# Kernel optimization log

Hardware: AMD Instinct MI355X
Metric: run time of the kernel (lower is better)

The kernel has to match this reference:

```python
import jax, jax.numpy as jnp
import numpy as np

D_MODEL = 768
N_HEADS = 12
D_K = D_MODEL // N_HEADS
NEG = -1e9


def setup_inputs() -> dict:
    key = jax.random.key(0)
    ks = jax.random.split(key, 10)
    B, S = 2, 2048
    x = jax.random.normal(ks[0], (B, S, D_MODEL), dtype=jnp.float32)
    # causal mask, broadcastable over batch and heads
    mask = jnp.tril(jnp.ones((S, S), dtype=jnp.int32))[None, None]
    scale = 1.0 / np.sqrt(D_MODEL)
    def lin(k):
        return jax.random.normal(k, (D_MODEL, D_MODEL), dtype=jnp.float32) * scale
    return {
        "x": x, "mask": mask,
        "wq": lin(ks[1]), "bq": jnp.zeros((D_MODEL,), jnp.float32),
        "wk": lin(ks[2]), "bk": jnp.zeros((D_MODEL,), jnp.float32),
        "wv": lin(ks[3]), "bv": jnp.zeros((D_MODEL,), jnp.float32),
        "wo": lin(ks[4]), "bo": jnp.zeros((D_MODEL,), jnp.float32),
    }


def reference(x, mask, wq, bq, wk, bk, wv, bv, wo, bo):
    B, S, _ = x.shape
    def split_heads(t):  # [B,S,D] -> [B,H,S,dk]
        return t.reshape(B, S, N_HEADS, D_K).transpose(0, 2, 1, 3)
    q = split_heads(x @ wq + bq)
    k = split_heads(x @ wk + bk)
    v = split_heads(x @ wv + bv)
    scores = jnp.einsum("bhqd,bhkd->bhqk", q, k) / jnp.sqrt(jnp.float32(D_K))
    scores = jnp.where(mask == 0, NEG, scores)
    attn = jax.nn.softmax(scores, axis=-1)
    # dropout is identity in eval mode
    ctx = jnp.einsum("bhqk,bhkd->bhqd", attn, v)
    ctx = ctx.transpose(0, 2, 1, 3).reshape(B, S, D_MODEL)
    return ctx @ wo + bo
```

## Files before the change

kernel.cpp:

```cpp
#include <hip/hip_runtime.h>
#include <hip/hip_bf16.h>
#include <stdint.h>

#define DM   768
#define NH   12
#define DKH  64
#define BB   2
#define SS   2048
#define MT   (BB*SS)
#define NQKV (3*DM)

typedef __attribute__((ext_vector_type(8))) short short8;
typedef __attribute__((ext_vector_type(4))) float f32x4;

__device__ __forceinline__ unsigned short f2bf(float f) {
    union { float f; unsigned u; } v; v.f = f;
    unsigned r = v.u + 0x7fffu + ((v.u >> 16) & 1u);
    return (unsigned short)(r >> 16);
}

__device__ __forceinline__ void gload_lds16(const unsigned short* g, unsigned short* l) {
    __builtin_amdgcn_global_load_lds((const __attribute__((address_space(1))) void*)g,
                                     (__attribute__((address_space(3))) void*)l, 16, 0, 0);
}

__launch_bounds__(256)
__global__ void k_conv(const float* __restrict__ x, unsigned short* __restrict__ xb,
                       const float* __restrict__ wq, const float* __restrict__ wk,
                       const float* __restrict__ wv, const float* __restrict__ wo,
                       unsigned short* __restrict__ wT) {
    __shared__ float tile[32][33];
    const int t = threadIdx.x;
    if (blockIdx.x < 3072) {
        int i = blockIdx.x * 256 + t;
        const float4 v = ((const float4*)x)[i];
        ushort4 o;
        o.x = f2bf(v.x); o.y = f2bf(v.y); o.z = f2bf(v.z); o.w = f2bf(v.w);
        ((ushort4*)xb)[i] = o;
    } else {
        const int cid = blockIdx.x - 3072;
        const int sel = cid / 576;
        const int rem = cid - sel * 576;
        const int kb = rem / 24, nb = rem - (rem / 24) * 24;
        const float* w = (sel == 0) ? wq : (sel == 1) ? wk : (sel == 2) ? wv : wo;
        const int k0 = kb * 32, n0 = nb * 32;
        const int tx = t & 31, ty = t >> 5;
        #pragma unroll
        for (int j = 0; j < 4; j++)
            tile[ty + 8*j][tx] = w[(size_t)(k0 + ty + 8*j) * DM + n0 + tx];
        __syncthreads();
        #pragma unroll
        for (int j = 0; j < 4; j++)
            wT[(size_t)(sel*DM + n0 + ty + 8*j) * DM + k0 + tx] = f2bf(tile[tx][ty + 8*j]);
    }
}

__launch_bounds__(256, 3)
__global__ void k_gemm_qkv(const unsigned short* __restrict__ xb,
                           const unsigned short* __restrict__ wT,
                           const float* __restrict__ bq, const float* __restrict__ bk,
                           const float* __restrict__ bv,
                           unsigned short* __restrict__ Qb,
                           unsigned short* __restrict__ Kb,
                           unsigned short* __restrict__ Vt) {
    __shared__ __align__(16) unsigned short Sh[128*128];
    unsigned short* As = Sh;
    unsigned short* Bs = Sh + 128*64;
    const int t = threadIdx.x;
    const int m0 = blockIdx.x * 128;
    const int n0 = blockIdx.y * 128;
    const int wid = t >> 6, lane = t & 63, q4 = lane >> 4, l16 = lane & 15;
    const int wm = (wid >> 1) * 64, wn = (wid & 1) * 64;

    const int srow = lane >> 3;
    const int scol = ((lane & 7) ^ srow) * 8;
    const unsigned short* Ag = xb + (size_t)(m0 + wid*8 + srow) * DM + scol;
    const unsigned short* Bg = wT + (size_t)(n0 + wid*8 + srow) * DM + scol;
    unsigned short* ldsA = &As[(wid*8)*64];
    unsigned short* ldsB = &Bs[(wid*8)*64];
    const int swz = (l16 & 7) * 8;

    f32x4 acc[4][4];
    for (int i = 0; i < 4; i++) for (int j = 0; j < 4; j++)
        acc[i][j] = (f32x4){0.f, 0.f, 0.f, 0.f};

    for (int kt = 0; kt < DM; kt += 64) {
        #pragma unroll
        for (int j = 0; j < 4; j++) {
            gload_lds16(Ag + (size_t)(j*32) * DM + kt, ldsA + j*32*64);
            gload_lds16(Bg + (size_t)(j*32) * DM + kt, ldsB + j*32*64);
        }
        __syncthreads();
        #pragma unroll
        for (int kc = 0; kc < 2; kc++) {
            short8 af[4], bf[4];
            #pragma unroll
            for (int i = 0; i < 4; i++)
                af[i] = *(const short8*)&As[(wm + i*16 + l16)*64 + ((kc*32 + q4*8) ^ swz)];
            #pragma unroll
            for (int i = 0; i < 4; i++)
                bf[i] = *(const short8*)&Bs[(wn + i*16 + l16)*64 + ((kc*32 + q4*8) ^ swz)];
            #pragma unroll
            for (int mi = 0; mi < 4; mi++)
                #pragma unroll
                for (int ni = 0; ni < 4; ni++)
                    acc[mi][ni] = __builtin_amdgcn_mfma_f32_16x16x32_bf16(af[mi], bf[ni], acc[mi][ni], 0, 0, 0);
        }
        __syncthreads();
    }

    const int sel = n0 / DM;
    if (sel < 2) {
        const float* bias = (sel == 0) ? bq : bk;
        for (int ni = 0; ni < 4; ni++) {
            const int col = n0 + wn + ni*16 + l16;
            const int c = col - sel * DM;
            const float bsv = bias[c];
            const int h = c >> 6, d = c & 63;
            for (int mi = 0; mi < 4; mi++) {
                for (int r = 0; r < 4; r++) {
                    const int row = m0 + wm + mi*16 + q4*4 + r;
                    const int b = row >> 11, s = row & 2047;
                    const int bh = b * NH + h;
                    float v = acc[mi][ni][r] + bsv;
                    if (sel == 0) Qb[(bh*SS + s)*DKH + d] = f2bf(v * 0.18033688011112042f);
                    else          Kb[(bh*SS + s)*DKH + d] = f2bf(v);
                }
            }
        }
    } else {
        const int cbase = n0 - 2*DM;
        const int bb = m0 >> 11, sbase = m0 & 2047;
        #pragma unroll
        for (int ni = 0; ni < 4; ni++) {
            const int c = wn + ni*16 + l16;
            const float bsv = bv[cbase + c];
            #pragma unroll
            for (int mi = 0; mi < 4; mi++) {
                const int rowb = wm + mi*16 + q4*4;
                ushort4 o;
                o.x = f2bf(acc[mi][ni][0] + bsv);
                o.y = f2bf(acc[mi][ni][1] + bsv);
                o.z = f2bf(acc[mi][ni][2] + bsv);
                o.w = f2bf(acc[mi][ni][3] + bsv);
                *(ushort4*)&Sh[c*128 + (rowb ^ ((c & 7) * 8))] = o;
            }
        }
        __syncthreads();
        const int dr = t >> 1, sq = (t & 1) * 64;
        const int hh = (cbase + dr) >> 6, d = (cbase + dr) & 63;
        const int bh = bb * NH + hh;
        unsigned short* Vg = Vt + ((size_t)bh*DKH + d)*SS + sbase + sq;
        #pragma unroll
        for (int j = 0; j < 8; j++) {
            short8 v = *(const short8*)&Sh[dr*128 + ((sq + j*8) ^ ((dr & 7) * 8))];
            *(short8*)&Vg[j*8] = v;
        }
    }
}

__device__ const int UNITS[48] = {
  (15<<16)|(0<<8)|16, (31<<16)|(0<<8)|16, (31<<16)|(16<<8)|32, (30<<16)|(0<<8)|16,
  (14<<16)|(0<<8)|15, (29<<16)|(0<<8)|15, (29<<16)|(15<<8)|30, (28<<16)|(0<<8)|15, (30<<16)|(16<<8)|31,
  (13<<16)|(0<<8)|14, (27<<16)|(0<<8)|14, (27<<16)|(14<<8)|28, (26<<16)|(0<<8)|14, (28<<16)|(15<<8)|29,
  (12<<16)|(0<<8)|13, (25<<16)|(0<<8)|13, (25<<16)|(13<<8)|26, (24<<16)|(0<<8)|13, (26<<16)|(14<<8)|27,
  (11<<16)|(0<<8)|12, (23<<16)|(0<<8)|12, (23<<16)|(12<<8)|24, (22<<16)|(0<<8)|12, (24<<16)|(13<<8)|25,
  (10<<16)|(0<<8)|11, (21<<16)|(0<<8)|11, (21<<16)|(11<<8)|22, (20<<16)|(0<<8)|11, (22<<16)|(12<<8)|23,
  ( 9<<16)|(0<<8)|10, (19<<16)|(0<<8)|10, (19<<16)|(10<<8)|20, (18<<16)|(0<<8)|10, (20<<16)|(11<<8)|21,
  ( 8<<16)|(0<<8)| 9, (17<<16)|(0<<8)| 9, (17<<16)|( 9<<8)|18, (16<<16)|(0<<8)| 9, (18<<16)|(10<<8)|19,
  ( 7<<16)|(0<<8)| 8, (16<<16)|( 9<<8)|17,
  ( 6<<16)|(0<<8)| 7, ( 5<<16)|(0<<8)| 6, ( 4<<16)|(0<<8)| 5, ( 3<<16)|(0<<8)| 4,
  ( 2<<16)|(0<<8)| 3, ( 1<<16)|(0<<8)| 2, ( 0<<16)|(0<<8)| 1,
};

__launch_bounds__(256, 4)
__global__ void k_attn(const unsigned short* __restrict__ Qb,
                       const unsigned short* __restrict__ Kb,
                       const unsigned short* __restrict__ Vt,
                       unsigned short* __restrict__ ctx,
                       float* __restrict__ Opart, float* __restrict__ lpart) {
    __shared__ __align__(16) unsigned short Ks[2][64*64];
    __shared__ __align__(16) unsigned short Vs[2][64*64];
    const int t = threadIdx.x;
    const int wid = t >> 6, lane = t & 63, q4 = lane >> 4, l16 = lane & 15;

    const int lin = blockIdx.x;
    const int bh = lin % 24;
    const int info = UNITS[lin / 24];
    const int qblk = info >> 16, t0 = (info >> 8) & 0xff, t1 = info & 0xff;
    const int b = bh / NH, h = bh - b * NH;
    const int qw = qblk * 64 + wid * 16;

    const unsigned short* Qp = Qb + (size_t)bh * SS * DKH;
    const unsigned short* Kp = Kb + (size_t)bh * SS * DKH;
    const unsigned short* Vp = Vt + (size_t)bh * DKH * SS;

    const int grow = lane >> 3;
    const int gcol = ((lane & 7) ^ grow) * 8;
    const int swz  = (l16 & 7) * 8;

    short8 qf[2];
    qf[0] = *(const short8*)(Qp + (size_t)(qw + l16)*DKH +      q4*8);
    qf[1] = *(const short8*)(Qp + (size_t)(qw + l16)*DKH + 32 + q4*8);

    const short8 ones = (short8){(short)0x3F80, (short)0x3F80, (short)0x3F80, (short)0x3F80,
                                 (short)0x3F80, (short)0x3F80, (short)0x3F80, (short)0x3F80};

    f32x4 accO[4];
    #pragma unroll
    for (int j = 0; j < 4; j++) accO[j] = (f32x4){0.f, 0.f, 0.f, 0.f};
    f32x4 accL = (f32x4){0.f, 0.f, 0.f, 0.f};

    {
        const int kb0 = t0 * 64;
        #pragma unroll
        for (int jj = 0; jj < 2; jj++) {
            const int r0 = wid*16 + jj*8;
            gload_lds16(Kp + (size_t)(kb0 + r0 + grow)*DKH + gcol, &Ks[0][r0*64]);
            gload_lds16(Vp + (size_t)(r0 + grow)*SS + kb0 + gcol,  &Vs[0][r0*64]);
        }
    }
    asm volatile("s_waitcnt vmcnt(0)" ::: "memory");
    __syncthreads();

    for (int kt = t0; kt < t1; kt++) {
        const int cb = (kt - t0) & 1, nb = cb ^ 1;
        const bool hasN = (kt + 1 < t1);
        if (hasN) {
            const int kn = (kt + 1) * 64;
            #pragma unroll
            for (int jj = 0; jj < 2; jj++) {
                const int r0 = wid*16 + jj*8;
                gload_lds16(Kp + (size_t)(kn + r0 + grow)*DKH + gcol, &Ks[nb][r0*64]);
                gload_lds16(Vp + (size_t)(r0 + grow)*SS + kn + gcol,  &Vs[nb][r0*64]);
            }
        }
        f32x4 St[4];
        #pragma unroll
        for (int ni = 0; ni < 4; ni++) St[ni] = (f32x4){0.f, 0.f, 0.f, 0.f};
        __builtin_amdgcn_s_setprio(1);
        #pragma unroll
        for (int ni = 0; ni < 4; ni++) {
            const int rbase = (ni*16 + l16) * 64;
            short8 kf0 = *(const short8*)&Ks[cb][rbase + ((     q4*8) ^ swz)];
            short8 kf1 = *(const short8*)&Ks[cb][rbase + ((32 + q4*8) ^ swz)];
            St[ni] = __builtin_amdgcn_mfma_f32_16x16x32_bf16(kf0, qf[0], St[ni], 0, 0, 0);
            St[ni] = __builtin_amdgcn_mfma_f32_16x16x32_bf16(kf1, qf[1], St[ni], 0, 0, 0);
        }
        __builtin_amdgcn_s_setprio(0);
        float p[4][4];
        if (kt < qblk) {
            #pragma unroll
            for (int ni = 0; ni < 4; ni++)
                #pragma unroll
                for (int r = 0; r < 4; r++)
                    p[ni][r] = __builtin_amdgcn_exp2f(St[ni][r]);
        } else {
            const int qrow = qw + l16;
            #pragma unroll
            for (int ni = 0; ni < 4; ni++) {
                const int key0 = kt*64 + ni*16 + q4*4;
                #pragma unroll
                for (int r = 0; r < 4; r++)
                    p[ni][r] = (key0 + r > qrow) ? 0.f : __builtin_amdgcn_exp2f(St[ni][r]);
            }
        }
        union { short8 v; unsigned u[4]; } pf0, pf1;
        {
            union { __hip_bfloat162 v; unsigned u; } w;
            w.v = __float22bfloat162_rn(make_float2(p[0][0], p[0][1])); pf0.u[0] = w.u;
            w.v = __float22bfloat162_rn(make_float2(p[0][2], p[0][3])); pf0.u[1] = w.u;
            w.v = __float22bfloat162_rn(make_float2(p[1][0], p[1][1])); pf0.u[2] = w.u;
            w.v = __float22bfloat162_rn(make_float2(p[1][2], p[1][3])); pf0.u[3] = w.u;
            w.v = __float22bfloat162_rn(make_float2(p[2][0], p[2][1])); pf1.u[0] = w.u;
            w.v = __float22bfloat162_rn(make_float2(p[2][2], p[2][3])); pf1.u[1] = w.u;
            w.v = __float22bfloat162_rn(make_float2(p[3][0], p[3][1])); pf1.u[2] = w.u;
            w.v = __float22bfloat162_rn(make_float2(p[3][2], p[3][3])); pf1.u[3] = w.u;
        }
        __builtin_amdgcn_s_setprio(1);
        accL = __builtin_amdgcn_mfma_f32_16x16x32_bf16(ones, pf0.v, accL, 0, 0, 0);
        accL = __builtin_amdgcn_mfma_f32_16x16x32_bf16(ones, pf1.v, accL, 0, 0, 0);
        #pragma unroll
        for (int ndi = 0; ndi < 4; ndi++) {
            const int rbase = (ndi*16 + l16) * 64;
            union { short8 v; unsigned long long d[2]; } vf0, vf1;
            vf0.d[0] = *(const unsigned long long*)&Vs[cb][rbase + ((     q4*4) ^ swz)];
            vf0.d[1] = *(const unsigned long long*)&Vs[cb][rbase + ((16 + q4*4) ^ swz)];
            vf1.d[0] = *(const unsigned long long*)&Vs[cb][rbase + ((32 + q4*4) ^ swz)];
            vf1.d[1] = *(const unsigned long long*)&Vs[cb][rbase + ((48 + q4*4) ^ swz)];
            accO[ndi] = __builtin_amdgcn_mfma_f32_16x16x32_bf16(vf0.v, pf0.v, accO[ndi], 0, 0, 0);
            accO[ndi] = __builtin_amdgcn_mfma_f32_16x16x32_bf16(vf1.v, pf1.v, accO[ndi], 0, 0, 0);
        }
        __builtin_amdgcn_s_setprio(0);
        asm volatile("s_waitcnt vmcnt(0)" ::: "memory");
        __syncthreads();
    }

    const float l = accL[0];

    if (qblk < 16) {
        const float inv = 1.0f / l;
        const size_t row = (size_t)(b*SS + qw + l16);
        #pragma unroll
        for (int ndi = 0; ndi < 4; ndi++) {
            ushort4 o;
            o.x = f2bf(accO[ndi][0] * inv);
            o.y = f2bf(accO[ndi][1] * inv);
            o.z = f2bf(accO[ndi][2] * inv);
            o.w = f2bf(accO[ndi][3] * inv);
            *(ushort4*)&ctx[row*DM + h*64 + ndi*16 + q4*4] = o;
        }
    } else {
        const int pair  = bh * 16 + (qblk - 16);
        const int chunk = (t0 != 0);
        const int qloc  = wid * 16 + l16;
        float* Op = Opart + ((size_t)pair * 2 + chunk) * 4096;
        #pragma unroll
        for (int ndi = 0; ndi < 4; ndi++)
            *(f32x4*)&Op[qloc*64 + ndi*16 + q4*4] = accO[ndi];
        if (q4 == 0) lpart[pair*128 + chunk*64 + qloc] = l;
    }
}

__launch_bounds__(256)
__global__ void k_combine(const float* __restrict__ Opart,
                          const float* __restrict__ lpart,
                          unsigned short* __restrict__ ctx) {
    const int pair = blockIdx.x;
    const int bh = pair >> 4, qblk = 16 + (pair & 15);
    const int b = bh / NH, h = bh - b * NH;
    const int t = threadIdx.x;
    const int q = t >> 2, dg = (t & 3) * 16;
    const float* P0 = Opart + (size_t)pair * 2 * 4096;
    const float* P1 = P0 + 4096;
    const float* L0 = lpart + pair * 128;
    const float inv = 1.0f / (L0[q] + L0[64 + q]);
    const size_t row = (size_t)(b*SS + qblk*64 + q);
    #pragma unroll
    for (int i = 0; i < 4; i++) {
        f32x4 a = *(const f32x4*)&P0[q*64 + dg + i*4];
        f32x4 c = *(const f32x4*)&P1[q*64 + dg + i*4];
        ushort4 o;
        o.x = f2bf((a[0] + c[0]) * inv);
        o.y = f2bf((a[1] + c[1]) * inv);
        o.z = f2bf((a[2] + c[2]) * inv);
        o.w = f2bf((a[3] + c[3]) * inv);
        *(ushort4*)&ctx[row*DM + h*64 + dg + i*4] = o;
    }
}

__launch_bounds__(256, 4)
__global__ void k_gemm_proj(const unsigned short* __restrict__ ctx,
                            const unsigned short* __restrict__ woT,
                            const float* __restrict__ bo,
                            float* __restrict__ out) {
    __shared__ __align__(16) unsigned short As[64*64];
    __shared__ __align__(16) unsigned short Bs[64*64];
    const int t = threadIdx.x;
    const int m0 = blockIdx.x * 64;
    const int n0 = blockIdx.y * 64;
    const int wid = t >> 6, lane = t & 63, q4 = lane >> 4, l16 = lane & 15;
    const int wm = (wid >> 1) * 32, wn = (wid & 1) * 32;

    const int srow = lane >> 3;
    const int scol = ((lane & 7) ^ srow) * 8;
    const unsigned short* Ag = ctx + (size_t)(m0 + wid*8 + srow) * DM + scol;
    const unsigned short* Bg = woT + (size_t)(n0 + wid*8 + srow) * DM + scol;
    unsigned short* ldsA = &As[(wid*8)*64];
    unsigned short* ldsB = &Bs[(wid*8)*64];
    const int swz = (l16 & 7) * 8;

    f32x4 acc[2][2];
    for (int i = 0; i < 2; i++) for (int j = 0; j < 2; j++)
        acc[i][j] = (f32x4){0.f, 0.f, 0.f, 0.f};

    for (int kt = 0; kt < DM; kt += 64) {
        #pragma unroll
        for (int j = 0; j < 2; j++) {
            gload_lds16(Ag + (size_t)(j*32) * DM + kt, ldsA + j*32*64);
            gload_lds16(Bg + (size_t)(j*32) * DM + kt, ldsB + j*32*64);
        }
        __syncthreads();
        #pragma unroll
        for (int kc = 0; kc < 2; kc++) {
            short8 af[2], bf[2];
            #pragma unroll
            for (int i = 0; i < 2; i++)
                af[i] = *(const short8*)&As[(wm + i*16 + l16)*64 + ((kc*32 + q4*8) ^ swz)];
            #pragma unroll
            for (int i = 0; i < 2; i++)
                bf[i] = *(const short8*)&Bs[(wn + i*16 + l16)*64 + ((kc*32 + q4*8) ^ swz)];
            #pragma unroll
            for (int mi = 0; mi < 2; mi++)
                #pragma unroll
                for (int ni = 0; ni < 2; ni++)
                    acc[mi][ni] = __builtin_amdgcn_mfma_f32_16x16x32_bf16(af[mi], bf[ni], acc[mi][ni], 0, 0, 0);
        }
        __syncthreads();
    }

    for (int ni = 0; ni < 2; ni++) {
        const int col = n0 + wn + ni*16 + l16;
        const float bsv = bo[col];
        for (int mi = 0; mi < 2; mi++) {
            for (int r = 0; r < 4; r++) {
                const int row = m0 + wm + mi*16 + q4*4 + r;
                out[(size_t)row * DM + col] = acc[mi][ni][r] + bsv;
            }
        }
    }
}

extern "C" void kernel_launch(void* const* d_in, const int* in_sizes, int n_in,
                              void* d_out, int out_size, void* d_ws, size_t ws_size,
                              hipStream_t stream) {
    const float* x  = (const float*)d_in[0];
    const float* wq = (const float*)d_in[2];
    const float* bq = (const float*)d_in[3];
    const float* wk = (const float*)d_in[4];
    const float* bk = (const float*)d_in[5];
    const float* wv = (const float*)d_in[6];
    const float* bv = (const float*)d_in[7];
    const float* wo = (const float*)d_in[8];
    const float* bo = (const float*)d_in[9];
    float* out = (float*)d_out;

    unsigned short* xb  = (unsigned short*)d_ws;
    unsigned short* wT  = xb + (size_t)MT * DM;
    unsigned short* Qb  = wT + (size_t)4 * DM * DM;
    unsigned short* Kb  = Qb + (size_t)BB * NH * SS * DKH;
    unsigned short* Vt  = Kb + (size_t)BB * NH * SS * DKH;
    unsigned short* ctx = Vt + (size_t)BB * NH * SS * DKH;
    float* Opart = (float*)(ctx + (size_t)MT * DM);
    float* lpart = Opart + (size_t)768 * 4096;

    k_conv<<<3072 + 2304, 256, 0, stream>>>(x, xb, wq, wk, wv, wo, wT);
    dim3 g1(MT / 128, NQKV / 128);
    k_gemm_qkv<<<g1, 256, 0, stream>>>(xb, wT, bq, bk, bv, Qb, Kb, Vt);
    k_attn<<<dim3(1152), 256, 0, stream>>>(Qb, Kb, Vt, ctx, Opart, lpart);
    k_combine<<<dim3(384), 256, 0, stream>>>(Opart, lpart, ctx);
    dim3 g3(MT / 64, DM / 64);
    k_gemm_proj<<<g3, 256, 0, stream>>>(ctx, wT + (size_t)3 * DM * DM, bo, out);
}
```

Baseline: 158.4 us.

## Double-buffer LDS tiles in QKV and output projection GEMMs

Both GEMM kernels now keep two LDS buffers and issue the direct global-to-LDS loads for the next K tile before running the MFMAs on the current one. A vmcnt wait and a barrier at the end of each iteration make the prefetched tile visible. This aims to hide global load latency behind matrix math. In exchange LDS use per block doubles, so the launch-bounds occupancy hints drop from 3 to 2 and from 4 to 3 blocks per CU, which may reduce latency hiding across waves.

After: 162.4 us. 2.6% more time.

```diff
diff --git a/kernel.cpp b/kernel.cpp
--- a/kernel.cpp
+++ b/kernel.cpp
@@ -55,7 +55,7 @@
     }
 }
 
-__launch_bounds__(256, 3)
+__launch_bounds__(256, 2)
 __global__ void k_gemm_qkv(const unsigned short* __restrict__ xb,
                            const unsigned short* __restrict__ wT,
                            const float* __restrict__ bq, const float* __restrict__ bk,
@@ -63,9 +63,7 @@
                            unsigned short* __restrict__ Qb,
                            unsigned short* __restrict__ Kb,
                            unsigned short* __restrict__ Vt) {
-    __shared__ __align__(16) unsigned short Sh[128*128];
-    unsigned short* As = Sh;
-    unsigned short* Bs = Sh + 128*64;
+    __shared__ __align__(16) unsigned short Sh[4*128*64];
     const int t = threadIdx.x;
     const int m0 = blockIdx.x * 128;
     const int n0 = blockIdx.y * 128;
@@ -76,21 +74,35 @@
     const int scol = ((lane & 7) ^ srow) * 8;
     const unsigned short* Ag = xb + (size_t)(m0 + wid*8 + srow) * DM + scol;
     const unsigned short* Bg = wT + (size_t)(n0 + wid*8 + srow) * DM + scol;
-    unsigned short* ldsA = &As[(wid*8)*64];
-    unsigned short* ldsB = &Bs[(wid*8)*64];
+    const int ldsW = (wid*8)*64;
     const int swz = (l16 & 7) * 8;
 
     f32x4 acc[4][4];
     for (int i = 0; i < 4; i++) for (int j = 0; j < 4; j++)
         acc[i][j] = (f32x4){0.f, 0.f, 0.f, 0.f};
 
-    for (int kt = 0; kt < DM; kt += 64) {
+    {
         #pragma unroll
         for (int j = 0; j < 4; j++) {
-            gload_lds16(Ag + (size_t)(j*32) * DM + kt, ldsA + j*32*64);
-            gload_lds16(Bg + (size_t)(j*32) * DM + kt, ldsB + j*32*64);
-        }
-        __syncthreads();
+            gload_lds16(Ag + (size_t)(j*32) * DM, Sh + ldsW + j*32*64);
+            gload_lds16(Bg + (size_t)(j*32) * DM, Sh + 8192 + ldsW + j*32*64);
+        }
+    }
+    asm volatile("s_waitcnt vmcnt(0)" ::: "memory");
+    __syncthreads();
+
+    for (int kti = 0; kti < 12; kti++) {
+        const int cb = kti & 1, nb = cb ^ 1;
+        if (kti + 1 < 12) {
+            const int kn = (kti + 1) * 64;
+            #pragma unroll
+            for (int j = 0; j < 4; j++) {
+                gload_lds16(Ag + (size_t)(j*32) * DM + kn, Sh + nb*16384 + ldsW + j*32*64);
+                gload_lds16(Bg + (size_t)(j*32) * DM + kn, Sh + nb*16384 + 8192 + ldsW + j*32*64);
+            }
+        }
+        const unsigned short* As = Sh + cb*16384;
+        const unsigned short* Bs = As + 8192;
         #pragma unroll
         for (int kc = 0; kc < 2; kc++) {
             short8 af[4], bf[4];
@@ -106,6 +118,7 @@
                 for (int ni = 0; ni < 4; ni++)
                     acc[mi][ni] = __builtin_amdgcn_mfma_f32_16x16x32_bf16(af[mi], bf[ni], acc[mi][ni], 0, 0, 0);
         }
+        asm volatile("s_waitcnt vmcnt(0)" ::: "memory");
         __syncthreads();
     }
 
@@ -349,13 +362,12 @@
     }
 }
 
-__launch_bounds__(256, 4)
+__launch_bounds__(256, 3)
 __global__ void k_gemm_proj(const unsigned short* __restrict__ ctx,
                             const unsigned short* __restrict__ woT,
                             const float* __restrict__ bo,
                             float* __restrict__ out) {
-    __shared__ __align__(16) unsigned short As[64*64];
-    __shared__ __align__(16) unsigned short Bs[64*64];
+    __shared__ __align__(16) unsigned short Sh[4*64*64];
     const int t = threadIdx.x;
     const int m0 = blockIdx.x * 64;
     const int n0 = blockIdx.y * 64;
@@ -366,21 +378,35 @@
     const int scol = ((lane & 7) ^ srow) * 8;
     const unsigned short* Ag = ctx + (size_t)(m0 + wid*8 + srow) * DM + scol;
     const unsigned short* Bg = woT + (size_t)(n0 + wid*8 + srow) * DM + scol;
-    unsigned short* ldsA = &As[(wid*8)*64];
-    unsigned short* ldsB = &Bs[(wid*8)*64];
+    const int ldsW = (wid*8)*64;
     const int swz = (l16 & 7) * 8;
 
     f32x4 acc[2][2];
     for (int i = 0; i < 2; i++) for (int j = 0; j < 2; j++)
         acc[i][j] = (f32x4){0.f, 0.f, 0.f, 0.f};
 
-    for (int kt = 0; kt < DM; kt += 64) {
+    {
         #pragma unroll
         for (int j = 0; j < 2; j++) {
-            gload_lds16(Ag + (size_t)(j*32) * DM + kt, ldsA + j*32*64);
-            gload_lds16(Bg + (size_t)(j*32) * DM + kt, ldsB + j*32*64);
-        }
-        __syncthreads();
+            gload_lds16(Ag + (size_t)(j*32) * DM, Sh + ldsW + j*32*64);
+            gload_lds16(Bg + (size_t)(j*32) * DM, Sh + 4096 + ldsW + j*32*64);
+        }
+    }
+    asm volatile("s_waitcnt vmcnt(0)" ::: "memory");
+    __syncthreads();
+
+    for (int kti = 0; kti < 12; kti++) {
+        const int cb = kti & 1, nb = cb ^ 1;
+        if (kti + 1 < 12) {
+            const int kn = (kti + 1) * 64;
+            #pragma unroll
+            for (int j = 0; j < 2; j++) {
+                gload_lds16(Ag + (size_t)(j*32) * DM + kn, Sh + nb*8192 + ldsW + j*32*64);
+                gload_lds16(Bg + (size_t)(j*32) * DM + kn, Sh + nb*8192 + 4096 + ldsW + j*32*64);
+            }
+        }
+        const unsigned short* As = Sh + cb*8192;
+        const unsigned short* Bs = As + 4096;
         #pragma unroll
         for (int kc = 0; kc < 2; kc++) {
             short8 af[2], bf[2];
@@ -396,6 +422,7 @@
                 for (int ni = 0; ni < 2; ni++)
                     acc[mi][ni] = __builtin_amdgcn_mfma_f32_16x16x32_bf16(af[mi], bf[ni], acc[mi][ni], 0, 0, 0);
         }
+        asm volatile("s_waitcnt vmcnt(0)" ::: "memory");
         __syncthreads();
     }
 
```
